# Kernel tuning notes

Hardware: AMD Instinct MI355X
Metric: run time of the kernel (lower is better)

Reference implementation:

```python
import jax, jax.numpy as jnp
import numpy as np

EMB = 4096   # emb_size for c2=256 (per TransformerEncoderBlock mapping)
HEADS = 16
HDIM = EMB // HEADS  # 256
N = 25               # (h // (h//5))**2 patches
PATCH = 4            # h//5 with h=20
C = 256
HW = 20
LN_EPS = 1e-5


def _layernorm(x, g, b):
    m = jnp.mean(x, axis=-1, keepdims=True)
    v = jnp.var(x, axis=-1, keepdims=True)
    return (x - m) * jax.lax.rsqrt(v + LN_EPS) * g + b


def setup_inputs() -> dict:
    key = jax.random.key(0)
    ks = jax.random.split(key, 14)
    s = 0.02
    rn = lambda k, shape, sc=s: jax.random.normal(k, shape, jnp.float32) * sc
    return {
        "x": jax.random.normal(ks[0], (1, C, HW, HW), jnp.float32),
        # PatchEmbedding: Conv2d(C, EMB, k=4, s=4) + positions
        "pe_w": rn(ks[1], (EMB, C, PATCH, PATCH)),
        "pe_b": jnp.zeros((EMB,), jnp.float32),
        "pos": rn(ks[2], (N, EMB), 1.0),  # nn.Parameter(torch.randn(...))
        # shared LayerNorm (same module used twice per block)
        "ln_g": jnp.ones((EMB,), jnp.float32),
        "ln_b": jnp.zeros((EMB,), jnp.float32),
        # attention
        "qkv_w": rn(ks[3], (EMB, 3 * EMB)),
        "qkv_b": jnp.zeros((3 * EMB,), jnp.float32),
        "proj_w": rn(ks[4], (EMB, EMB)),
        "proj_b": jnp.zeros((EMB,), jnp.float32),
        # FFN (expansion 4)
        "ff1_w": rn(ks[5], (EMB, 4 * EMB)),
        "ff1_b": jnp.zeros((4 * EMB,), jnp.float32),
        "ff2_w": rn(ks[6], (4 * EMB, EMB)),
        "ff2_b": jnp.zeros((EMB,), jnp.float32),
    }


def _forward(x, pe_w, pe_b, pos, ln_g, ln_b, qkv_w, qkv_b, proj_w, proj_b,
             ff1_w, ff1_b, ff2_w, ff2_b):
    b = x.shape[0]
    # Patch embedding: Conv2d(k=4, s=4) -> [b, EMB, 5, 5] -> [b, 25, EMB]
    t = jax.lax.conv_general_dilated(
        x, pe_w, window_strides=(PATCH, PATCH), padding="VALID",
        dimension_numbers=("NCHW", "OIHW", "NCHW"))
    t = t + pe_b[None, :, None, None]
    t = t.reshape(b, EMB, N).transpose(0, 2, 1) + pos  # [b, N, EMB]

    # --- TransformerEncoderBlock (dropout inactive / eval mode) ---
    # attention branch
    h = _layernorm(t, ln_g, ln_b)
    qkv = (h @ qkv_w + qkv_b).reshape(b, N, HEADS, HDIM, 3)  # (h d qkv) split
    q = qkv[..., 0].transpose(0, 2, 1, 3)  # [b, H, N, D]
    k = qkv[..., 1].transpose(0, 2, 1, 3)
    v = qkv[..., 2].transpose(0, 2, 1, 3)
    energy = jnp.einsum("bhqd,bhkd->bhqk", q, k)
    # NOTE: original scales AFTER softmax by sqrt(emb_size) -- faithful copy
    att = jax.nn.softmax(energy, axis=-1) / (EMB ** 0.5)
    o = jnp.einsum("bhqk,bhkd->bhqd", att, v)
    o = o.transpose(0, 2, 1, 3).reshape(b, N, EMB)
    t = t + (o @ proj_w + proj_b)

    # FFN branch (same shared layernorm params)
    h = _layernorm(t, ln_g, ln_b)
    h = jax.nn.gelu(h @ ff1_w + ff1_b, approximate=False)  # torch nn.GELU exact
    t = t + (h @ ff2_w + ff2_b)

    # final reshape(1, c2, w, h)
    return t.reshape(1, C, HW, HW)


def reference(x, pe_w, pe_b, pos, ln_g, ln_b, qkv_w, qkv_b, proj_w, proj_b,
              ff1_w, ff1_b, ff2_w, ff2_b):
    return _forward(x, pe_w, pe_b, pos, ln_g, ln_b, qkv_w, qkv_b, proj_w,
                    proj_b, ff1_w, ff1_b, ff2_w, ff2_b)
```

## Files before the change

### kernel.cpp

```cpp
#include <hip/hip_runtime.h>
#include <math.h>

#define TOK 25

typedef __attribute__((ext_vector_type(8))) short short8_t;
typedef __attribute__((ext_vector_type(4))) float f32x4_t;
typedef __attribute__((ext_vector_type(8))) float floatx8;
typedef __attribute__((ext_vector_type(4))) float floatx4;
typedef __attribute__((ext_vector_type(8))) __bf16 bf16x8_t;
typedef __attribute__((ext_vector_type(4))) __bf16 bf16x4_t;

__device__ __forceinline__ short8_t cvt8(floatx8 f) {
  return __builtin_bit_cast(short8_t, __builtin_convertvector(f, bf16x8_t));
}
__device__ __forceinline__ uint2 cvt4pack(float4 v) {
  floatx4 f = {v.x, v.y, v.z, v.w};
  return __builtin_bit_cast(uint2, __builtin_convertvector(f, bf16x4_t));
}
__device__ __forceinline__ unsigned short bf1(float f) {
  return __builtin_bit_cast(unsigned short, (__bf16)f);
}

template <int KC, int WT>
__global__ __launch_bounds__(256) void k_mfma(
    const unsigned short* __restrict__ A, const float* __restrict__ W,
    float* __restrict__ part, int K, int N) {
  constexpr int LDA = KC + 8;
  __shared__ __align__(16) unsigned short As[TOK * LDA];
  const int tid = threadIdx.x;
  const int lane = tid & 63;
  const int lm = lane & 15;
  const int lg = lane >> 4;
  const int wv = tid >> 6;
  const int s = blockIdx.y;
  const int k0 = s * KC;
  const int c0 = blockIdx.x * 256 + wv * 64;
  for (int i = tid; i < TOK * (KC / 8); i += 256) {
    int r = i / (KC / 8);
    int o = i - r * (KC / 8);
    uint4 v = *reinterpret_cast<const uint4*>(A + (long)r * K + k0 + o * 8);
    *reinterpret_cast<uint4*>(&As[r * LDA + o * 8]) = v;
  }
  __syncthreads();
  const int r1 = 16 + lm;
  const int r1c = (r1 < TOK) ? r1 : 0;
  f32x4_t acc[4][2];
#pragma unroll
  for (int g = 0; g < 4; ++g) {
    acc[g][0] = (f32x4_t){0.f, 0.f, 0.f, 0.f};
    acc[g][1] = (f32x4_t){0.f, 0.f, 0.f, 0.f};
  }
  for (int ks = 0; ks < KC; ks += 32) {
    const int kb = k0 + ks + lg * 8;
    floatx8 bfv[4];
    if (WT == 0) {
      const float* bp = W + (long)kb * N + c0 + lm;
#pragma unroll
      for (int j = 0; j < 8; ++j) {
        const float* bj = bp + (long)j * N;
#pragma unroll
        for (int g = 0; g < 4; ++g) bfv[g][j] = bj[g * 16];
      }
    } else {
#pragma unroll
      for (int g = 0; g < 4; ++g) {
        const float* bp = W + (long)(c0 + g * 16 + lm) * K + kb;
        float4 b0 = *reinterpret_cast<const float4*>(bp);
        float4 b1 = *reinterpret_cast<const float4*>(bp + 4);
        bfv[g] = (floatx8){b0.x, b0.y, b0.z, b0.w, b1.x, b1.y, b1.z, b1.w};
      }
    }
    short8_t av0 =
        *reinterpret_cast<const short8_t*>(&As[lm * LDA + ks + lg * 8]);
    short8_t av1 =
        *reinterpret_cast<const short8_t*>(&As[r1c * LDA + ks + lg * 8]);
#pragma unroll
    for (int g = 0; g < 4; ++g) {
      short8_t bv = cvt8(bfv[g]);
      acc[g][0] = __builtin_amdgcn_mfma_f32_16x16x32_bf16(av0, bv, acc[g][0], 0, 0, 0);
      acc[g][1] = __builtin_amdgcn_mfma_f32_16x16x32_bf16(av1, bv, acc[g][1], 0, 0, 0);
    }
  }
  float* pp = part + ((long)s * TOK) * N + c0 + lm;
#pragma unroll
  for (int g = 0; g < 4; ++g) {
    float* pg = pp + g * 16;
#pragma unroll
    for (int r = 0; r < 4; ++r) {
      int row0 = lg * 4 + r;
      pg[(long)row0 * N] = acc[g][0][r];
      int row1 = 16 + lg * 4 + r;
      if (row1 < TOK) pg[(long)row1 * N] = acc[g][1][r];
    }
  }
}

template <int KC>
__global__ __launch_bounds__(256) void k_mfma_pe(
    const float* __restrict__ x, const float* __restrict__ W,
    float* __restrict__ part, int K, int N) {
  constexpr int LDA = KC + 8;
  __shared__ __align__(16) unsigned short As[TOK * LDA];
  const int tid = threadIdx.x;
  const int lane = tid & 63;
  const int lm = lane & 15;
  const int lg = lane >> 4;
  const int wv = tid >> 6;
  const int s = blockIdx.y;
  const int k0 = s * KC;
  const int c0 = blockIdx.x * 256 + wv * 64;
  for (int i = tid; i < TOK * (KC / 8); i += 256) {
    int r = i / (KC / 8);
    int o = i - r * (KC / 8);
    int kb = k0 + o * 8;
    int c = kb >> 4;
    int kh0 = (kb >> 2) & 3;
    int py = r / 5, px = r - py * 5;
    const float* xp = x + c * 400 + (py * 4 + kh0) * 20 + px * 4;
    float4 lo = *reinterpret_cast<const float4*>(xp);
    float4 hi = *reinterpret_cast<const float4*>(xp + 20);
    floatx8 f = {lo.x, lo.y, lo.z, lo.w, hi.x, hi.y, hi.z, hi.w};
    short8_t v = cvt8(f);
    *reinterpret_cast<short8_t*>(&As[r * LDA + o * 8]) = v;
  }
  __syncthreads();
  const int r1 = 16 + lm;
  const int r1c = (r1 < TOK) ? r1 : 0;
  f32x4_t acc[4][2];
#pragma unroll
  for (int g = 0; g < 4; ++g) {
    acc[g][0] = (f32x4_t){0.f, 0.f, 0.f, 0.f};
    acc[g][1] = (f32x4_t){0.f, 0.f, 0.f, 0.f};
  }
  for (int ks = 0; ks < KC; ks += 32) {
    const int kb = k0 + ks + lg * 8;
    floatx8 bfv[4];
#pragma unroll
    for (int g = 0; g < 4; ++g) {
      const float* bp = W + (long)(c0 + g * 16 + lm) * K + kb;
      float4 b0 = *reinterpret_cast<const float4*>(bp);
      float4 b1 = *reinterpret_cast<const float4*>(bp + 4);
      bfv[g] = (floatx8){b0.x, b0.y, b0.z, b0.w, b1.x, b1.y, b1.z, b1.w};
    }
    short8_t av0 =
        *reinterpret_cast<const short8_t*>(&As[lm * LDA + ks + lg * 8]);
    short8_t av1 =
        *reinterpret_cast<const short8_t*>(&As[r1c * LDA + ks + lg * 8]);
#pragma unroll
    for (int g = 0; g < 4; ++g) {
      short8_t bv = cvt8(bfv[g]);
      acc[g][0] = __builtin_amdgcn_mfma_f32_16x16x32_bf16(av0, bv, acc[g][0], 0, 0, 0);
      acc[g][1] = __builtin_amdgcn_mfma_f32_16x16x32_bf16(av1, bv, acc[g][1], 0, 0, 0);
    }
  }
  float* pp = part + ((long)s * TOK) * N + c0 + lm;
#pragma unroll
  for (int g = 0; g < 4; ++g) {
    float* pg = pp + g * 16;
#pragma unroll
    for (int r = 0; r < 4; ++r) {
      int row0 = lg * 4 + r;
      pg[(long)row0 * N] = acc[g][0][r];
      int row1 = 16 + lg * 4 + r;
      if (row1 < TOK) pg[(long)row1 * N] = acc[g][1][r];
    }
  }
}

template <int S, int GELU, int RES, int OBF>
__global__ __launch_bounds__(256) void k_reduce(const float* __restrict__ part,
                                                const float* __restrict__ bias,
                                                const float* __restrict__ res,
                                                void* __restrict__ outv,
                                                int Nout) {
  long idx4 = (long)blockIdx.x * 256 + threadIdx.x;
  int c4 = (int)(idx4 % (Nout >> 2));
  const long stride4 = (long)TOK * (Nout >> 2);
  const float4* p4 = reinterpret_cast<const float4*>(part) + idx4;
  float4 v = {0.f, 0.f, 0.f, 0.f};
#pragma unroll
  for (int s = 0; s < S; ++s) {
    float4 t = p4[s * stride4];
    v.x += t.x; v.y += t.y; v.z += t.z; v.w += t.w;
  }
  float4 bb = reinterpret_cast<const float4*>(bias)[c4];
  v.x += bb.x; v.y += bb.y; v.z += bb.z; v.w += bb.w;
  if (GELU) {
    v.x = 0.5f * v.x * (1.f + erff(v.x * 0.70710678118654752f));
    v.y = 0.5f * v.y * (1.f + erff(v.y * 0.70710678118654752f));
    v.z = 0.5f * v.z * (1.f + erff(v.z * 0.70710678118654752f));
    v.w = 0.5f * v.w * (1.f + erff(v.w * 0.70710678118654752f));
  }
  if (RES) {
    float4 rr = reinterpret_cast<const float4*>(res)[idx4];
    v.x += rr.x; v.y += rr.y; v.z += rr.z; v.w += rr.w;
  }
  if (OBF) {
    reinterpret_cast<uint2*>(outv)[idx4] = cvt4pack(v);
  } else {
    reinterpret_cast<float4*>(outv)[idx4] = v;
  }
}

__global__ __launch_bounds__(256) void k_ln(const float* __restrict__ t,
                                            const float* __restrict__ g,
                                            const float* __restrict__ b,
                                            unsigned short* __restrict__ h) {
  const int n = blockIdx.x;
  const float4* row = reinterpret_cast<const float4*>(t + n * 4096);
  float s = 0.f, s2 = 0.f;
  float4 vbuf[4];
#pragma unroll
  for (int it = 0; it < 4; ++it) {
    float4 v = row[threadIdx.x + it * 256];
    vbuf[it] = v;
    s += v.x + v.y + v.z + v.w;
    s2 += v.x * v.x + v.y * v.y + v.z * v.z + v.w * v.w;
  }
#pragma unroll
  for (int off = 32; off >= 1; off >>= 1) {
    s += __shfl_down(s, off);
    s2 += __shfl_down(s2, off);
  }
  __shared__ float red[8];
  if ((threadIdx.x & 63) == 0) {
    red[threadIdx.x >> 6] = s;
    red[4 + (threadIdx.x >> 6)] = s2;
  }
  __syncthreads();
  float st = red[0] + red[1] + red[2] + red[3];
  float s2t = red[4] + red[5] + red[6] + red[7];
  float mean = st * (1.f / 4096.f);
  float var = s2t * (1.f / 4096.f) - mean * mean;
  float rstd = rsqrtf(var + 1e-5f);
  const float4* g4 = reinterpret_cast<const float4*>(g);
  const float4* b4 = reinterpret_cast<const float4*>(b);
  uint2* h2 = reinterpret_cast<uint2*>(h) + (long)n * 1024;
#pragma unroll
  for (int it = 0; it < 4; ++it) {
    int i = threadIdx.x + it * 256;
    float4 v = vbuf[it];
    float4 gg = g4[i];
    float4 bb = b4[i];
    float4 o;
    o.x = (v.x - mean) * rstd * gg.x + bb.x;
    o.y = (v.y - mean) * rstd * gg.y + bb.y;
    o.z = (v.z - mean) * rstd * gg.z + bb.z;
    o.w = (v.w - mean) * rstd * gg.w + bb.w;
    h2[i] = cvt4pack(o);
  }
}

__global__ __launch_bounds__(256) void k_attn(const float* __restrict__ qkv,
                                              unsigned short* __restrict__ o) {
  const int head = blockIdx.x;
  __shared__ float q[TOK][260];
  __shared__ float kk[TOK][260];
  __shared__ float att[TOK][TOK];
  const int d = threadIdx.x;
#pragma unroll
  for (int n = 0; n < TOK; ++n) {
    const long base = (long)n * 12288 + (head * 256 + d) * 3;
    q[n][d] = qkv[base];
    kk[n][d] = qkv[base + 1];
  }
  __syncthreads();
  for (int p = threadIdx.x; p < TOK * TOK; p += 256) {
    int i = p / TOK, j = p - i * TOK;
    float acc = 0.f;
#pragma unroll
    for (int c = 0; c < 256; c += 4) {
      float4 a = *reinterpret_cast<const float4*>(&q[i][c]);
      float4 bb = *reinterpret_cast<const float4*>(&kk[j][c]);
      acc = fmaf(a.x, bb.x, acc);
      acc = fmaf(a.y, bb.y, acc);
      acc = fmaf(a.z, bb.z, acc);
      acc = fmaf(a.w, bb.w, acc);
    }
    att[i][j] = acc;
  }
  __syncthreads();
  if (threadIdx.x < TOK) {
    const int i = threadIdx.x;
    float m = -1e30f;
    for (int j = 0; j < TOK; ++j) m = fmaxf(m, att[i][j]);
    float ssum = 0.f;
    float ex[TOK];
#pragma unroll
    for (int j = 0; j < TOK; ++j) {
      ex[j] = expf(att[i][j] - m);
      ssum += ex[j];
    }
    float inv = 1.f / (ssum * 64.f);
#pragma unroll
    for (int j = 0; j < TOK; ++j) att[i][j] = ex[j] * inv;
  }
  __syncthreads();
  float acc[TOK];
#pragma unroll
  for (int i = 0; i < TOK; ++i) acc[i] = 0.f;
#pragma unroll
  for (int j = 0; j < TOK; ++j) {
    float vv = qkv[(long)j * 12288 + (head * 256 + d) * 3 + 2];
#pragma unroll
    for (int i = 0; i < TOK; ++i) acc[i] = fmaf(att[i][j], vv, acc[i]);
  }
#pragma unroll
  for (int i = 0; i < TOK; ++i)
    o[(long)i * 4096 + head * 256 + d] = bf1(acc[i]);
}

extern "C" void kernel_launch(void* const* d_in, const int* in_sizes, int n_in,
                              void* d_out, int out_size, void* d_ws, size_t ws_size,
                              hipStream_t stream) {
  (void)in_sizes; (void)n_in; (void)out_size; (void)ws_size;
  const float* x      = (const float*)d_in[0];
  const float* pe_w   = (const float*)d_in[1];
  const float* pe_b   = (const float*)d_in[2];
  const float* pos    = (const float*)d_in[3];
  const float* ln_g   = (const float*)d_in[4];
  const float* ln_b   = (const float*)d_in[5];
  const float* qkv_w  = (const float*)d_in[6];
  const float* qkv_b  = (const float*)d_in[7];
  const float* proj_w = (const float*)d_in[8];
  const float* proj_b = (const float*)d_in[9];
  const float* ff1_w  = (const float*)d_in[10];
  const float* ff1_b  = (const float*)d_in[11];
  const float* ff2_w  = (const float*)d_in[12];
  const float* ff2_b  = (const float*)d_in[13];
  float* out = (float*)d_out;

  float* ws = (float*)d_ws;
  float* T    = ws + 102400;
  unsigned short* H_bf = (unsigned short*)(ws + 204800);
  float* QKV  = ws + 307200;
  unsigned short* O_bf = (unsigned short*)(ws + 614400);
  unsigned short* G_bf = (unsigned short*)(ws + 716800);
  float* PART = ws + 1136400;

  k_mfma_pe<128><<<dim3(16, 32), 256, 0, stream>>>(x, pe_w, PART, 4096, 4096);
  k_reduce<32, 0, 1, 0><<<100, 256, 0, stream>>>(PART, pe_b, pos, T, 4096);
  k_ln<<<25, 256, 0, stream>>>(T, ln_g, ln_b, H_bf);

  k_mfma<256, 0><<<dim3(48, 16), 256, 0, stream>>>(H_bf, qkv_w, PART, 4096, 12288);
  k_reduce<16, 0, 0, 0><<<300, 256, 0, stream>>>(PART, qkv_b, nullptr, QKV, 12288);
  k_attn<<<16, 256, 0, stream>>>(QKV, O_bf);
  k_mfma<128, 0><<<dim3(16, 32), 256, 0, stream>>>(O_bf, proj_w, PART, 4096, 4096);
  k_reduce<32, 0, 1, 0><<<100, 256, 0, stream>>>(PART, proj_b, T, T, 4096);
  k_ln<<<25, 256, 0, stream>>>(T, ln_g, ln_b, H_bf);

  k_mfma<256, 0><<<dim3(64, 16), 256, 0, stream>>>(H_bf, ff1_w, PART, 4096, 16384);
  k_reduce<16, 1, 0, 1><<<400, 256, 0, stream>>>(PART, ff1_b, nullptr, G_bf, 16384);
  k_mfma<512, 0><<<dim3(16, 32), 256, 0, stream>>>(G_bf, ff2_w, PART, 16384, 4096);
  k_reduce<32, 0, 1, 0><<<100, 256, 0, stream>>>(PART, ff2_b, T, out, 4096);
}
```

Measured before the change: 243.3 us.

## Fuse LayerNorm into reduce stats and GEMM prologue, prefetch weight tiles

Removes the two standalone LayerNorm launches. The preceding split-K reduce now accumulates per-row sum and sum-of-squares with atomics, and the following GEMM normalizes its fp32 activation tile while staging it into shared memory. The weight-load loop is also software-pipelined by double-buffering the next K-step in registers. The trade-offs are a memset launch, atomic contention, redundant normalization work across blocks, extra register pressure from the prefetch buffer, and slightly different variance rounding.

```diff
diff --git a/kernel.cpp b/kernel.cpp
--- a/kernel.cpp
+++ b/kernel.cpp
@@ -21,12 +21,14 @@
   return __builtin_bit_cast(unsigned short, (__bf16)f);
 }
 
-template <int KC, int WT>
+template <int KC, int WT, int LN>
 __global__ __launch_bounds__(256) void k_mfma(
-    const unsigned short* __restrict__ A, const float* __restrict__ W,
-    float* __restrict__ part, int K, int N) {
+    const void* __restrict__ Av, const float* __restrict__ W,
+    const float* __restrict__ stats, const float* __restrict__ lng,
+    const float* __restrict__ lnb, float* __restrict__ part, int K, int N) {
   constexpr int LDA = KC + 8;
   __shared__ __align__(16) unsigned short As[TOK * LDA];
+  __shared__ float ms[TOK], rs[TOK];
   const int tid = threadIdx.x;
   const int lane = tid & 63;
   const int lm = lane & 15;
@@ -35,11 +37,40 @@
   const int s = blockIdx.y;
   const int k0 = s * KC;
   const int c0 = blockIdx.x * 256 + wv * 64;
+  if (LN) {
+    if (tid < TOK) {
+      float s1 = stats[tid * 2], s2 = stats[tid * 2 + 1];
+      float mean = s1 * (1.f / 4096.f);
+      float var = s2 * (1.f / 4096.f) - mean * mean;
+      ms[tid] = mean;
+      rs[tid] = rsqrtf(var + 1e-5f);
+    }
+    __syncthreads();
+  }
   for (int i = tid; i < TOK * (KC / 8); i += 256) {
     int r = i / (KC / 8);
     int o = i - r * (KC / 8);
-    uint4 v = *reinterpret_cast<const uint4*>(A + (long)r * K + k0 + o * 8);
-    *reinterpret_cast<uint4*>(&As[r * LDA + o * 8]) = v;
+    if (LN) {
+      const float* tp = (const float*)Av + (long)r * K + k0 + o * 8;
+      float4 lo = *reinterpret_cast<const float4*>(tp);
+      float4 hi = *reinterpret_cast<const float4*>(tp + 4);
+      const float* gp = lng + k0 + o * 8;
+      const float* bp = lnb + k0 + o * 8;
+      float4 g0 = *reinterpret_cast<const float4*>(gp);
+      float4 g1 = *reinterpret_cast<const float4*>(gp + 4);
+      float4 b0 = *reinterpret_cast<const float4*>(bp);
+      float4 b1 = *reinterpret_cast<const float4*>(bp + 4);
+      float m = ms[r], rr = rs[r];
+      floatx8 f = {(lo.x - m) * rr * g0.x + b0.x, (lo.y - m) * rr * g0.y + b0.y,
+                   (lo.z - m) * rr * g0.z + b0.z, (lo.w - m) * rr * g0.w + b0.w,
+                   (hi.x - m) * rr * g1.x + b1.x, (hi.y - m) * rr * g1.y + b1.y,
+                   (hi.z - m) * rr * g1.z + b1.z, (hi.w - m) * rr * g1.w + b1.w};
+      *reinterpret_cast<short8_t*>(&As[r * LDA + o * 8]) = cvt8(f);
+    } else {
+      uint4 v = *reinterpret_cast<const uint4*>((const unsigned short*)Av +
+                                                (long)r * K + k0 + o * 8);
+      *reinterpret_cast<uint4*>(&As[r * LDA + o * 8]) = v;
+    }
   }
   __syncthreads();
   const int r1 = 16 + lm;
@@ -50,16 +81,15 @@
     acc[g][0] = (f32x4_t){0.f, 0.f, 0.f, 0.f};
     acc[g][1] = (f32x4_t){0.f, 0.f, 0.f, 0.f};
   }
-  for (int ks = 0; ks < KC; ks += 32) {
+  auto loadW = [&](int ks, floatx8(&dst)[4]) {
     const int kb = k0 + ks + lg * 8;
-    floatx8 bfv[4];
     if (WT == 0) {
       const float* bp = W + (long)kb * N + c0 + lm;
 #pragma unroll
       for (int j = 0; j < 8; ++j) {
         const float* bj = bp + (long)j * N;
 #pragma unroll
-        for (int g = 0; g < 4; ++g) bfv[g][j] = bj[g * 16];
+        for (int g = 0; g < 4; ++g) dst[g][j] = bj[g * 16];
       }
     } else {
 #pragma unroll
@@ -67,18 +97,27 @@
         const float* bp = W + (long)(c0 + g * 16 + lm) * K + kb;
         float4 b0 = *reinterpret_cast<const float4*>(bp);
         float4 b1 = *reinterpret_cast<const float4*>(bp + 4);
-        bfv[g] = (floatx8){b0.x, b0.y, b0.z, b0.w, b1.x, b1.y, b1.z, b1.w};
+        dst[g] = (floatx8){b0.x, b0.y, b0.z, b0.w, b1.x, b1.y, b1.z, b1.w};
       }
     }
+  };
+  floatx8 wcur[4], wnxt[4];
+  loadW(0, wcur);
+  for (int ks = 0; ks < KC; ks += 32) {
+    if (ks + 32 < KC) loadW(ks + 32, wnxt);
     short8_t av0 =
         *reinterpret_cast<const short8_t*>(&As[lm * LDA + ks + lg * 8]);
     short8_t av1 =
         *reinterpret_cast<const short8_t*>(&As[r1c * LDA + ks + lg * 8]);
 #pragma unroll
     for (int g = 0; g < 4; ++g) {
-      short8_t bv = cvt8(bfv[g]);
+      short8_t bv = cvt8(wcur[g]);
       acc[g][0] = __builtin_amdgcn_mfma_f32_16x16x32_bf16(av0, bv, acc[g][0], 0, 0, 0);
       acc[g][1] = __builtin_amdgcn_mfma_f32_16x16x32_bf16(av1, bv, acc[g][1], 0, 0, 0);
+    }
+    if (ks + 32 < KC) {
+#pragma unroll
+      for (int g = 0; g < 4; ++g) wcur[g] = wnxt[g];
     }
   }
   float* pp = part + ((long)s * TOK) * N + c0 + lm;
@@ -120,8 +159,7 @@
     float4 lo = *reinterpret_cast<const float4*>(xp);
     float4 hi = *reinterpret_cast<const float4*>(xp + 20);
     floatx8 f = {lo.x, lo.y, lo.z, lo.w, hi.x, hi.y, hi.z, hi.w};
-    short8_t v = cvt8(f);
-    *reinterpret_cast<short8_t*>(&As[r * LDA + o * 8]) = v;
+    *reinterpret_cast<short8_t*>(&As[r * LDA + o * 8]) = cvt8(f);
   }
   __syncthreads();
   const int r1 = 16 + lm;
@@ -167,13 +205,15 @@
   }
 }
 
-template <int S, int GELU, int RES, int OBF>
+template <int S, int GELU, int RES, int OBF, int STATS>
 __global__ __launch_bounds__(256) void k_reduce(const float* __restrict__ part,
                                                 const float* __restrict__ bias,
                                                 const float* __restrict__ res,
                                                 void* __restrict__ outv,
+                                                float* __restrict__ stats,
                                                 int Nout) {
-  long idx4 = (long)blockIdx.x * 256 + threadIdx.x;
+  const int tid = threadIdx.x;
+  long idx4 = (long)blockIdx.x * 256 + tid;
   int c4 = (int)(idx4 % (Nout >> 2));
   const long stride4 = (long)TOK * (Nout >> 2);
   const float4* p4 = reinterpret_cast<const float4*>(part) + idx4;
@@ -200,54 +240,25 @@
   } else {
     reinterpret_cast<float4*>(outv)[idx4] = v;
   }
-}
-
-__global__ __launch_bounds__(256) void k_ln(const float* __restrict__ t,
-                                            const float* __restrict__ g,
-                                            const float* __restrict__ b,
-                                            unsigned short* __restrict__ h) {
-  const int n = blockIdx.x;
-  const float4* row = reinterpret_cast<const float4*>(t + n * 4096);
-  float s = 0.f, s2 = 0.f;
-  float4 vbuf[4];
-#pragma unroll
-  for (int it = 0; it < 4; ++it) {
-    float4 v = row[threadIdx.x + it * 256];
-    vbuf[it] = v;
-    s += v.x + v.y + v.z + v.w;
-    s2 += v.x * v.x + v.y * v.y + v.z * v.z + v.w * v.w;
-  }
-#pragma unroll
-  for (int off = 32; off >= 1; off >>= 1) {
-    s += __shfl_down(s, off);
-    s2 += __shfl_down(s2, off);
-  }
-  __shared__ float red[8];
-  if ((threadIdx.x & 63) == 0) {
-    red[threadIdx.x >> 6] = s;
-    red[4 + (threadIdx.x >> 6)] = s2;
-  }
-  __syncthreads();
-  float st = red[0] + red[1] + red[2] + red[3];
-  float s2t = red[4] + red[5] + red[6] + red[7];
-  float mean = st * (1.f / 4096.f);
-  float var = s2t * (1.f / 4096.f) - mean * mean;
-  float rstd = rsqrtf(var + 1e-5f);
-  const float4* g4 = reinterpret_cast<const float4*>(g);
-  const float4* b4 = reinterpret_cast<const float4*>(b);
-  uint2* h2 = reinterpret_cast<uint2*>(h) + (long)n * 1024;
-#pragma unroll
-  for (int it = 0; it < 4; ++it) {
-    int i = threadIdx.x + it * 256;
-    float4 v = vbuf[it];
-    float4 gg = g4[i];
-    float4 bb = b4[i];
-    float4 o;
-    o.x = (v.x - mean) * rstd * gg.x + bb.x;
-    o.y = (v.y - mean) * rstd * gg.y + bb.y;
-    o.z = (v.z - mean) * rstd * gg.z + bb.z;
-    o.w = (v.w - mean) * rstd * gg.w + bb.w;
-    h2[i] = cvt4pack(o);
+  if (STATS) {
+    float s1 = v.x + v.y + v.z + v.w;
+    float s2 = v.x * v.x + v.y * v.y + v.z * v.z + v.w * v.w;
+#pragma unroll
+    for (int off = 32; off >= 1; off >>= 1) {
+      s1 += __shfl_down(s1, off);
+      s2 += __shfl_down(s2, off);
+    }
+    __shared__ float red[8];
+    if ((tid & 63) == 0) {
+      red[tid >> 6] = s1;
+      red[4 + (tid >> 6)] = s2;
+    }
+    __syncthreads();
+    if (tid == 0) {
+      int row = blockIdx.x >> 2;
+      atomicAdd(&stats[row * 2], red[0] + red[1] + red[2] + red[3]);
+      atomicAdd(&stats[row * 2 + 1], red[4] + red[5] + red[6] + red[7]);
+    }
   }
 }
 
@@ -332,25 +343,32 @@
 
   float* ws = (float*)d_ws;
   float* T    = ws + 102400;
-  unsigned short* H_bf = (unsigned short*)(ws + 204800);
   float* QKV  = ws + 307200;
   unsigned short* O_bf = (unsigned short*)(ws + 614400);
   unsigned short* G_bf = (unsigned short*)(ws + 716800);
+  float* STATS0 = ws + 1126400;
+  float* STATS1 = ws + 1126464;
   float* PART = ws + 1136400;
 
+  hipMemsetAsync(STATS0, 0, 128 * sizeof(float), stream);
+
   k_mfma_pe<128><<<dim3(16, 32), 256, 0, stream>>>(x, pe_w, PART, 4096, 4096);
-  k_reduce<32, 0, 1, 0><<<100, 256, 0, stream>>>(PART, pe_b, pos, T, 4096);
-  k_ln<<<25, 256, 0, stream>>>(T, ln_g, ln_b, H_bf);
-
-  k_mfma<256, 0><<<dim3(48, 16), 256, 0, stream>>>(H_bf, qkv_w, PART, 4096, 12288);
-  k_reduce<16, 0, 0, 0><<<300, 256, 0, stream>>>(PART, qkv_b, nullptr, QKV, 12288);
+  k_reduce<32, 0, 1, 0, 1><<<100, 256, 0, stream>>>(PART, pe_b, pos, T, STATS0, 4096);
+
+  k_mfma<256, 0, 1><<<dim3(48, 16), 256, 0, stream>>>(T, qkv_w, STATS0, ln_g, ln_b,
+                                                      PART, 4096, 12288);
+  k_reduce<16, 0, 0, 0, 0><<<300, 256, 0, stream>>>(PART, qkv_b, nullptr, QKV,
+                                                    nullptr, 12288);
   k_attn<<<16, 256, 0, stream>>>(QKV, O_bf);
-  k_mfma<128, 0><<<dim3(16, 32), 256, 0, stream>>>(O_bf, proj_w, PART, 4096, 4096);
-  k_reduce<32, 0, 1, 0><<<100, 256, 0, stream>>>(PART, proj_b, T, T, 4096);
-  k_ln<<<25, 256, 0, stream>>>(T, ln_g, ln_b, H_bf);
-
-  k_mfma<256, 0><<<dim3(64, 16), 256, 0, stream>>>(H_bf, ff1_w, PART, 4096, 16384);
-  k_reduce<16, 1, 0, 1><<<400, 256, 0, stream>>>(PART, ff1_b, nullptr, G_bf, 16384);
-  k_mfma<512, 0><<<dim3(16, 32), 256, 0, stream>>>(G_bf, ff2_w, PART, 16384, 4096);
-  k_reduce<32, 0, 1, 0><<<100, 256, 0, stream>>>(PART, ff2_b, T, out, 4096);
-}
+  k_mfma<128, 0, 0><<<dim3(16, 32), 256, 0, stream>>>(O_bf, proj_w, nullptr, nullptr,
+                                                      nullptr, PART, 4096, 4096);
+  k_reduce<32, 0, 1, 0, 1><<<100, 256, 0, stream>>>(PART, proj_b, T, T, STATS1, 4096);
+
+  k_mfma<256, 0, 1><<<dim3(64, 16), 256, 0, stream>>>(T, ff1_w, STATS1, ln_g, ln_b,
+                                                      PART, 4096, 16384);
+  k_reduce<16, 1, 0, 1, 0><<<400, 256, 0, stream>>>(PART, ff1_b, nullptr, G_bf,
+                                                    nullptr, 16384);
+  k_mfma<512, 0, 0><<<dim3(16, 32), 256, 0, stream>>>(G_bf, ff2_w, nullptr, nullptr,
+                                                      nullptr, PART, 16384, 4096);
+  k_reduce<32, 0, 1, 0, 0><<<100, 256, 0, stream>>>(PART, ff2_b, T, out, nullptr, 4096);
+}
```

Measured after the change: 250.8 us. +3.1%, slower.

## Store split-K partials as bf16 in MFMA fragment layout and prefetch weights

Applied to the files above, without the earlier changes.

Split-K GEMM kernels now write partial sums as packed bf16 in the native MFMA accumulator layout (one uint2 per lane) instead of scattered fp32 row-major stores. The reduce kernel is rewritten to decode that layout, sum in fp32, and scatter results to row-major outputs. This halves partial-buffer traffic. The k_mfma weight loads are also double-buffered in registers so the next K-step's loads overlap the MFMAs. Rounding each partial to bf16 before summation loses precision, and the padded rows 25..31 add some wasted traffic.

```diff
diff --git a/kernel.cpp b/kernel.cpp
--- a/kernel.cpp
+++ b/kernel.cpp
@@ -17,14 +17,19 @@
   floatx4 f = {v.x, v.y, v.z, v.w};
   return __builtin_bit_cast(uint2, __builtin_convertvector(f, bf16x4_t));
 }
+__device__ __forceinline__ uint2 pack4(f32x4_t v) {
+  floatx4 f = {v[0], v[1], v[2], v[3]};
+  return __builtin_bit_cast(uint2, __builtin_convertvector(f, bf16x4_t));
+}
 __device__ __forceinline__ unsigned short bf1(float f) {
   return __builtin_bit_cast(unsigned short, (__bf16)f);
 }
+
 
 template <int KC, int WT>
 __global__ __launch_bounds__(256) void k_mfma(
     const unsigned short* __restrict__ A, const float* __restrict__ W,
-    float* __restrict__ part, int K, int N) {
+    uint2* __restrict__ part, int K, int N) {
   constexpr int LDA = KC + 8;
   __shared__ __align__(16) unsigned short As[TOK * LDA];
   const int tid = threadIdx.x;
@@ -50,16 +55,15 @@
     acc[g][0] = (f32x4_t){0.f, 0.f, 0.f, 0.f};
     acc[g][1] = (f32x4_t){0.f, 0.f, 0.f, 0.f};
   }
-  for (int ks = 0; ks < KC; ks += 32) {
+  auto loadW = [&](int ks, floatx8(&dst)[4]) {
     const int kb = k0 + ks + lg * 8;
-    floatx8 bfv[4];
     if (WT == 0) {
       const float* bp = W + (long)kb * N + c0 + lm;
 #pragma unroll
       for (int j = 0; j < 8; ++j) {
         const float* bj = bp + (long)j * N;
 #pragma unroll
-        for (int g = 0; g < 4; ++g) bfv[g][j] = bj[g * 16];
+        for (int g = 0; g < 4; ++g) dst[g][j] = bj[g * 16];
       }
     } else {
 #pragma unroll
@@ -67,38 +71,42 @@
         const float* bp = W + (long)(c0 + g * 16 + lm) * K + kb;
         float4 b0 = *reinterpret_cast<const float4*>(bp);
         float4 b1 = *reinterpret_cast<const float4*>(bp + 4);
-        bfv[g] = (floatx8){b0.x, b0.y, b0.z, b0.w, b1.x, b1.y, b1.z, b1.w};
+        dst[g] = (floatx8){b0.x, b0.y, b0.z, b0.w, b1.x, b1.y, b1.z, b1.w};
       }
     }
+  };
+  floatx8 wcur[4], wnxt[4];
+  loadW(0, wcur);
+  for (int ks = 0; ks < KC; ks += 32) {
+    if (ks + 32 < KC) loadW(ks + 32, wnxt);
     short8_t av0 =
         *reinterpret_cast<const short8_t*>(&As[lm * LDA + ks + lg * 8]);
     short8_t av1 =
         *reinterpret_cast<const short8_t*>(&As[r1c * LDA + ks + lg * 8]);
 #pragma unroll
     for (int g = 0; g < 4; ++g) {
-      short8_t bv = cvt8(bfv[g]);
+      short8_t bv = cvt8(wcur[g]);
       acc[g][0] = __builtin_amdgcn_mfma_f32_16x16x32_bf16(av0, bv, acc[g][0], 0, 0, 0);
       acc[g][1] = __builtin_amdgcn_mfma_f32_16x16x32_bf16(av1, bv, acc[g][1], 0, 0, 0);
     }
-  }
-  float* pp = part + ((long)s * TOK) * N + c0 + lm;
+    if (ks + 32 < KC) {
+#pragma unroll
+      for (int g = 0; g < 4; ++g) wcur[g] = wnxt[g];
+    }
+  }
+  const long sbase = (long)s * N * 8;
 #pragma unroll
   for (int g = 0; g < 4; ++g) {
-    float* pg = pp + g * 16;
-#pragma unroll
-    for (int r = 0; r < 4; ++r) {
-      int row0 = lg * 4 + r;
-      pg[(long)row0 * N] = acc[g][0][r];
-      int row1 = 16 + lg * 4 + r;
-      if (row1 < TOK) pg[(long)row1 * N] = acc[g][1][r];
-    }
+    long t = ((long)(c0 >> 4) + g) * 128;
+    part[sbase + t + lane] = pack4(acc[g][0]);
+    part[sbase + t + 64 + lane] = pack4(acc[g][1]);
   }
 }
 
 template <int KC>
 __global__ __launch_bounds__(256) void k_mfma_pe(
     const float* __restrict__ x, const float* __restrict__ W,
-    float* __restrict__ part, int K, int N) {
+    uint2* __restrict__ part, int K, int N) {
   constexpr int LDA = KC + 8;
   __shared__ __align__(16) unsigned short As[TOK * LDA];
   const int tid = threadIdx.x;
@@ -120,8 +128,7 @@
     float4 lo = *reinterpret_cast<const float4*>(xp);
     float4 hi = *reinterpret_cast<const float4*>(xp + 20);
     floatx8 f = {lo.x, lo.y, lo.z, lo.w, hi.x, hi.y, hi.z, hi.w};
-    short8_t v = cvt8(f);
-    *reinterpret_cast<short8_t*>(&As[r * LDA + o * 8]) = v;
+    *reinterpret_cast<short8_t*>(&As[r * LDA + o * 8]) = cvt8(f);
   }
   __syncthreads();
   const int r1 = 16 + lm;
@@ -153,52 +160,57 @@
       acc[g][1] = __builtin_amdgcn_mfma_f32_16x16x32_bf16(av1, bv, acc[g][1], 0, 0, 0);
     }
   }
-  float* pp = part + ((long)s * TOK) * N + c0 + lm;
+  const long sbase = (long)s * N * 8;
 #pragma unroll
   for (int g = 0; g < 4; ++g) {
-    float* pg = pp + g * 16;
-#pragma unroll
-    for (int r = 0; r < 4; ++r) {
-      int row0 = lg * 4 + r;
-      pg[(long)row0 * N] = acc[g][0][r];
-      int row1 = 16 + lg * 4 + r;
-      if (row1 < TOK) pg[(long)row1 * N] = acc[g][1][r];
-    }
+    long t = ((long)(c0 >> 4) + g) * 128;
+    part[sbase + t + lane] = pack4(acc[g][0]);
+    part[sbase + t + 64 + lane] = pack4(acc[g][1]);
   }
 }
 
 template <int S, int GELU, int RES, int OBF>
-__global__ __launch_bounds__(256) void k_reduce(const float* __restrict__ part,
+__global__ __launch_bounds__(256) void k_reduce(const uint2* __restrict__ part,
                                                 const float* __restrict__ bias,
                                                 const float* __restrict__ res,
                                                 void* __restrict__ outv,
                                                 int Nout) {
-  long idx4 = (long)blockIdx.x * 256 + threadIdx.x;
-  int c4 = (int)(idx4 % (Nout >> 2));
-  const long stride4 = (long)TOK * (Nout >> 2);
-  const float4* p4 = reinterpret_cast<const float4*>(part) + idx4;
-  float4 v = {0.f, 0.f, 0.f, 0.f};
+  const long gidx = (long)blockIdx.x * 256 + threadIdx.x;
+  const int lane = (int)(gidx & 63);
+  const int half = (int)((gidx >> 6) & 1);
+  const long ct = gidx >> 7;
+  const int lm = lane & 15, lg = lane >> 4;
+  const int col = (int)(ct * 16 + lm);
+  const long stride = (long)Nout * 8;
+  const uint2* pp = part + gidx;
+  float a[4] = {0.f, 0.f, 0.f, 0.f};
 #pragma unroll
   for (int s = 0; s < S; ++s) {
-    float4 t = p4[s * stride4];
-    v.x += t.x; v.y += t.y; v.z += t.z; v.w += t.w;
-  }
-  float4 bb = reinterpret_cast<const float4*>(bias)[c4];
-  v.x += bb.x; v.y += bb.y; v.z += bb.z; v.w += bb.w;
-  if (GELU) {
-    v.x = 0.5f * v.x * (1.f + erff(v.x * 0.70710678118654752f));
-    v.y = 0.5f * v.y * (1.f + erff(v.y * 0.70710678118654752f));
-    v.z = 0.5f * v.z * (1.f + erff(v.z * 0.70710678118654752f));
-    v.w = 0.5f * v.w * (1.f + erff(v.w * 0.70710678118654752f));
-  }
-  if (RES) {
-    float4 rr = reinterpret_cast<const float4*>(res)[idx4];
-    v.x += rr.x; v.y += rr.y; v.z += rr.z; v.w += rr.w;
-  }
-  if (OBF) {
-    reinterpret_cast<uint2*>(outv)[idx4] = cvt4pack(v);
-  } else {
-    reinterpret_cast<float4*>(outv)[idx4] = v;
+    uint2 u = pp[(long)s * stride];
+    a[0] += __builtin_bit_cast(float, (u.x & 0xffffu) << 16);
+    a[1] += __builtin_bit_cast(float, u.x & 0xffff0000u);
+    a[2] += __builtin_bit_cast(float, (u.y & 0xffffu) << 16);
+    a[3] += __builtin_bit_cast(float, u.y & 0xffff0000u);
+  }
+  const float bb = bias[col];
+#pragma unroll
+  for (int r = 0; r < 4; ++r) {
+    a[r] += bb;
+    if (GELU) a[r] = 0.5f * a[r] * (1.f + erff(a[r] * 0.70710678118654752f));
+  }
+  const int row0 = half * 16 + lg * 4;
+#pragma unroll
+  for (int r = 0; r < 4; ++r) {
+    int row = row0 + r;
+    if (row < TOK) {
+      float v = a[r];
+      if (RES) v += res[(long)row * Nout + col];
+      if (OBF) {
+        ((unsigned short*)outv)[(long)row * Nout + col] = bf1(v);
+      } else {
+        ((float*)outv)[(long)row * Nout + col] = v;
+      }
+    }
   }
 }
 
@@ -336,21 +348,21 @@
   float* QKV  = ws + 307200;
   unsigned short* O_bf = (unsigned short*)(ws + 614400);
   unsigned short* G_bf = (unsigned short*)(ws + 716800);
-  float* PART = ws + 1136400;
+  uint2* PART = (uint2*)(ws + 1136400);
 
   k_mfma_pe<128><<<dim3(16, 32), 256, 0, stream>>>(x, pe_w, PART, 4096, 4096);
-  k_reduce<32, 0, 1, 0><<<100, 256, 0, stream>>>(PART, pe_b, pos, T, 4096);
+  k_reduce<32, 0, 1, 0><<<128, 256, 0, stream>>>(PART, pe_b, pos, T, 4096);
   k_ln<<<25, 256, 0, stream>>>(T, ln_g, ln_b, H_bf);
 
   k_mfma<256, 0><<<dim3(48, 16), 256, 0, stream>>>(H_bf, qkv_w, PART, 4096, 12288);
-  k_reduce<16, 0, 0, 0><<<300, 256, 0, stream>>>(PART, qkv_b, nullptr, QKV, 12288);
+  k_reduce<16, 0, 0, 0><<<384, 256, 0, stream>>>(PART, qkv_b, nullptr, QKV, 12288);
   k_attn<<<16, 256, 0, stream>>>(QKV, O_bf);
   k_mfma<128, 0><<<dim3(16, 32), 256, 0, stream>>>(O_bf, proj_w, PART, 4096, 4096);
-  k_reduce<32, 0, 1, 0><<<100, 256, 0, stream>>>(PART, proj_b, T, T, 4096);
+  k_reduce<32, 0, 1, 0><<<128, 256, 0, stream>>>(PART, proj_b, T, T, 4096);
   k_ln<<<25, 256, 0, stream>>>(T, ln_g, ln_b, H_bf);
 
   k_mfma<256, 0><<<dim3(64, 16), 256, 0, stream>>>(H_bf, ff1_w, PART, 4096, 16384);
-  k_reduce<16, 1, 0, 1><<<400, 256, 0, stream>>>(PART, ff1_b, nullptr, G_bf, 16384);
+  k_reduce<16, 1, 0, 1><<<512, 256, 0, stream>>>(PART, ff1_b, nullptr, G_bf, 16384);
   k_mfma<512, 0><<<dim3(16, 32), 256, 0, stream>>>(G_bf, ff2_w, PART, 16384, 4096);
-  k_reduce<32, 0, 1, 0><<<100, 256, 0, stream>>>(PART, ff2_b, T, out, 4096);
-}
+  k_reduce<32, 0, 1, 0><<<128, 256, 0, stream>>>(PART, ff2_b, T, out, 4096);
+}
```

After: 234.0 us. -3.8%, faster.
